# Kernel optimization log

Hardware: AMD Instinct MI355X
Metric: run time of the kernel (lower is better)

The kernel has to match this reference:

```python
import jax, jax.numpy as jnp
import numpy as np

N = 100000   # nodes
E = 1600000  # edges
IN = 32      # in_channels
ED = 16      # edge_dim
G = 128      # num graphs in batch
NEG = 0.01   # LeakyReLU default slope

def lrelu(v):
    return jnp.where(v > 0, v, NEG * v)

def gine_conv(x, src, dst, edge_attr, We, be, Wa, ba, Wb, bb):
    # PyG GINEConv (eps=0): out = nn(x + sum_{j->i} relu(x_j + lin(edge_attr)))
    e = edge_attr @ We + be                      # [E, d]
    m = jax.nn.relu(x[src] + e)                  # gather + add + relu
    agg = jax.ops.segment_sum(m, dst, num_segments=x.shape[0])
    h = x + agg
    return lrelu(h @ Wa + ba) @ Wb + bb

def setup_inputs() -> dict:
    key = jax.random.key(0)
    ks = jax.random.split(key, 24)
    w = lambda k, shape: (jax.random.normal(k, shape, dtype=jnp.float32) * 0.05)
    inp = {
        "x": jax.random.normal(ks[0], (N, IN), dtype=jnp.float32),
        "edge_index": jax.random.randint(ks[1], (2, E), 0, N),
        "edge_attr": jax.random.normal(ks[2], (E, ED), dtype=jnp.float32),
        "batch": jnp.sort(jax.random.randint(ks[3], (N,), 0, G)),
        # conv1: edge lin ED->IN, nn IN->32->64
        "We1": w(ks[4], (ED, IN)), "be1": w(ks[5], (IN,)),
        "W1a": w(ks[6], (IN, 32)), "b1a": w(ks[7], (32,)),
        "W1b": w(ks[8], (32, 64)), "b1b": w(ks[9], (64,)),
        # conv2: edge lin ED->64, nn 64->128->256
        "We2": w(ks[10], (ED, 64)), "be2": w(ks[11], (64,)),
        "W2a": w(ks[12], (64, 128)), "b2a": w(ks[13], (128,)),
        "W2b": w(ks[14], (128, 256)), "b2b": w(ks[15], (256,)),
        # head
        "Wf0": w(ks[16], (256, 128)), "bf0": w(ks[17], (128,)),
        "Wf1": w(ks[18], (128, 64)), "bf1": w(ks[19], (64,)),
        "Wf2": w(ks[20], (64, 32)), "bf2": w(ks[21], (32,)),
        "Wr": w(ks[22], (32, 1)), "br": w(ks[23], (1,)),
    }
    return inp

def reference(x, edge_index, edge_attr, batch,
              We1, be1, W1a, b1a, W1b, b1b,
              We2, be2, W2a, b2a, W2b, b2b,
              Wf0, bf0, Wf1, bf1, Wf2, bf2, Wr, br):
    src, dst = edge_index[0], edge_index[1]
    h = gine_conv(x, src, dst, edge_attr, We1, be1, W1a, b1a, W1b, b1b)
    h = lrelu(h)
    h = gine_conv(h, src, dst, edge_attr, We2, be2, W2a, b2a, W2b, b2b)
    h = lrelu(h)
    # global_add_pool over graph ids
    g = jax.ops.segment_sum(h, batch, num_segments=G)   # [G, 256]
    g = lrelu(g @ Wf0 + bf0)
    # dropout: identity (inference reference)
    g = lrelu(g @ Wf1 + bf1)
    g = lrelu(g @ Wf2 + bf2)
    out = (g @ Wr + br)[:, 0]                           # squeeze(dim=1)
    return out
```

## Files before the change

### kernel.cpp

```cpp
#include <hip/hip_runtime.h>

__device__ __forceinline__ float lrelu(float v){ return v > 0.f ? v : 0.01f*v; }

typedef __attribute__((ext_vector_type(8))) short v8s;
typedef __attribute__((ext_vector_type(4))) float v4f;

__device__ __forceinline__ unsigned short f2bf(float f){
    union{float f; unsigned int i;} v; v.f = f;
    unsigned int u = v.i;
    return (unsigned short)((u + 0x7fffu + ((u >> 16) & 1u)) >> 16);
}
__device__ __forceinline__ unsigned int pack2(float a, float b){
    return (unsigned int)f2bf(a) | ((unsigned int)f2bf(b) << 16);
}
__device__ __forceinline__ float bflo(unsigned int u){
    union{unsigned int i; float f;} v; v.i = u << 16; return v.f;
}
__device__ __forceinline__ float bfhi(unsigned int u){
    union{unsigned int i; float f;} v; v.i = u & 0xffff0000u; return v.f;
}
__device__ __forceinline__ float bf2f(unsigned short s){
    union{unsigned int i; float f;} v; v.i = ((unsigned int)s) << 16; return v.f;
}

__global__ __launch_bounds__(256) void k_hist(
    const int* __restrict__ ei, int* __restrict__ deg, int E)
{
    int e = blockIdx.x * 256 + threadIdx.x;
    if (e >= E) return;
    atomicAdd(&deg[ei[E + e]], 1);
}

__global__ __launch_bounds__(256) void k_scan1(
    const int* __restrict__ deg, int* __restrict__ rowptr,
    int* __restrict__ bsum, int N)
{
    __shared__ int sh[256];
    int t = threadIdx.x;
    int i = blockIdx.x * 256 + t;
    int v = (i < N) ? deg[i] : 0;
    sh[t] = v;
    __syncthreads();
    #pragma unroll
    for (int off = 1; off < 256; off <<= 1) {
        int add = (t >= off) ? sh[t - off] : 0;
        __syncthreads();
        sh[t] += add;
        __syncthreads();
    }
    if (i < N) rowptr[i] = sh[t] - v;
    if (t == 255) bsum[blockIdx.x] = sh[t];
}

__global__ __launch_bounds__(512) void k_scan2(int* __restrict__ bsum, int nb)
{
    __shared__ int sh[512];
    int t = threadIdx.x;
    int v = (t < nb) ? bsum[t] : 0;
    sh[t] = v;
    __syncthreads();
    #pragma unroll
    for (int off = 1; off < 512; off <<= 1) {
        int add = (t >= off) ? sh[t - off] : 0;
        __syncthreads();
        sh[t] += add;
        __syncthreads();
    }
    if (t < nb) bsum[t] = sh[t] - v;
}

__global__ __launch_bounds__(256) void k_scan3(
    int* __restrict__ rowptr, int* __restrict__ cursor,
    const int* __restrict__ bsum, int N)
{
    int i = blockIdx.x * 256 + threadIdx.x;
    if (i >= N) return;
    int rp = rowptr[i] + bsum[i >> 8];
    rowptr[i] = rp;
    cursor[i] = rp;
}

__global__ __launch_bounds__(256) void k_castx(
    const float* __restrict__ x, unsigned int* __restrict__ xb, int M8)
{
    int i = blockIdx.x * 256 + threadIdx.x;
    if (i >= M8) return;
    const float4* p = reinterpret_cast<const float4*>(x) + (size_t)i * 2;
    float4 a = p[0], b = p[1];
    uint4 o;
    o.x = pack2(a.x, a.y); o.y = pack2(a.z, a.w);
    o.z = pack2(b.x, b.y); o.w = pack2(b.z, b.w);
    reinterpret_cast<uint4*>(xb)[i] = o;
}

__global__ __launch_bounds__(256) void k_castw(
    const float* __restrict__ W2a, const float* __restrict__ W2b,
    const float* __restrict__ We1, const float* __restrict__ We2,
    unsigned short* __restrict__ W2aT, unsigned short* __restrict__ W2bT,
    unsigned short* __restrict__ WeT1, unsigned short* __restrict__ WeT2)
{
    int i = blockIdx.x * 256 + threadIdx.x;
    if (i < 128 * 64) {
        int n = i >> 6, k = i & 63;
        W2aT[i] = f2bf(W2a[k * 128 + n]);
    }
    int j = i - 128 * 64;
    if (j >= 0 && j < 256 * 128) {
        int n = j >> 7, k = j & 127;
        W2bT[j] = f2bf(W2b[k * 256 + n]);
    }
    int q1 = i - (128 * 64 + 256 * 128);
    if (q1 >= 0 && q1 < 32 * 32) {
        int cch = q1 >> 5, k = q1 & 31;
        WeT1[q1] = (k < 16) ? f2bf(We1[k * 32 + cch]) : (unsigned short)0;
    }
    int q2 = q1 - 32 * 32;
    if (q2 >= 0 && q2 < 64 * 32) {
        int cch = q2 >> 5, k = q2 & 31;
        WeT2[q2] = (k < 16) ? f2bf(We2[k * 64 + cch]) : (unsigned short)0;
    }
}

__global__ __launch_bounds__(256) void k_scatter(
    const int* __restrict__ ei, const float* __restrict__ ea,
    int* __restrict__ cursor, int2* __restrict__ csr2,
    uint4* __restrict__ eab, int E)
{
    int e = blockIdx.x * 256 + threadIdx.x;
    if (e >= E) return;
    int s = ei[e];
    int d = ei[E + e];
    int slot = atomicAdd(&cursor[d], 1);
    const float4* p = reinterpret_cast<const float4*>(ea) + (size_t)e * 4;
    float4 a = p[0], b = p[1], c = p[2], f = p[3];
    uint4 o0, o1;
    o0.x = pack2(a.x, a.y); o0.y = pack2(a.z, a.w);
    o0.z = pack2(b.x, b.y); o0.w = pack2(b.z, b.w);
    o1.x = pack2(c.x, c.y); o1.y = pack2(c.z, c.w);
    o1.z = pack2(f.x, f.y); o1.w = pack2(f.z, f.w);
    eab[(size_t)slot * 2]     = o0;
    eab[(size_t)slot * 2 + 1] = o1;
    int2 r; r.x = s; r.y = d;
    csr2[slot] = r;
}

#define AGG_SPW 64

__global__ __launch_bounds__(256) void k_agg2(
    const unsigned short* __restrict__ xb,
    const uint4* __restrict__ eab,
    const unsigned short* __restrict__ WeT,
    const float* __restrict__ be,
    const int2* __restrict__ csr2, float* __restrict__ agg, int E)
{
    __shared__ __align__(16) float lds[4][2][16][68];
    const int tid  = threadIdx.x;
    const int wv   = tid >> 6;
    const int lane = tid & 63;
    const int lid  = lane & 15;
    const int quad = lane >> 4;
    const int wave = __builtin_amdgcn_readfirstlane((blockIdx.x * 256 + tid) >> 6);
    const int s0 = wave * AGG_SPW;
    if (s0 >= E) return;
    const int nsl = (s0 + AGG_SPW <= E) ? AGG_SPW : E - s0;

    v8s af0 = *reinterpret_cast<const v8s*>(WeT + lid * 32 + quad * 8);
    v8s af1 = *reinterpret_cast<const v8s*>(WeT + (16 + lid) * 32 + quad * 8);
    v8s af2 = *reinterpret_cast<const v8s*>(WeT + (32 + lid) * 32 + quad * 8);
    v8s af3 = *reinterpret_cast<const v8s*>(WeT + (48 + lid) * 32 + quad * 8);
    const float biasc = be[lane];
    const int2*  cp = csr2 + s0;
    const uint4* ep = eab + (size_t)s0 * 2;

    unsigned short xv[2][16];
    int dsv[2][16];
    float acc = 0.f;
    int   cur = cp[0].y;
    bool  owned = false;

    auto GATHER = [&](int t) {
        const int base = t * 16;
        const int cnt = nsl - base;
        #pragma unroll
        for (int e = 0; e < 16; ++e) {
            int ee = (e < cnt) ? e : cnt - 1;
            int2 r = cp[base + ee];
            dsv[t & 1][e] = r.y;
            xv[t & 1][e] = xb[(unsigned)r.x * 64u + (unsigned)lane];
        }
    };
    auto MFMA = [&](int t) {
        int sl = t * 16 + lid;
        if (sl > nsl - 1) sl = nsl - 1;
        uint4 bw = {0u, 0u, 0u, 0u};
        if (quad < 2) bw = ep[2 * sl + quad];
        union { uint4 u; v8s s; } uu; uu.u = bw;
        v8s bf = uu.s;
        v4f d0 = {0.f, 0.f, 0.f, 0.f}, d1 = d0, d2 = d0, d3 = d0;
        d0 = __builtin_amdgcn_mfma_f32_16x16x32_bf16(af0, bf, d0, 0, 0, 0);
        d1 = __builtin_amdgcn_mfma_f32_16x16x32_bf16(af1, bf, d1, 0, 0, 0);
        d2 = __builtin_amdgcn_mfma_f32_16x16x32_bf16(af2, bf, d2, 0, 0, 0);
        d3 = __builtin_amdgcn_mfma_f32_16x16x32_bf16(af3, bf, d3, 0, 0, 0);
        float* lp = &lds[wv][t & 1][lid][quad * 4];
        *reinterpret_cast<v4f*>(lp)      = d0;
        *reinterpret_cast<v4f*>(lp + 16) = d1;
        *reinterpret_cast<v4f*>(lp + 32) = d2;
        *reinterpret_cast<v4f*>(lp + 48) = d3;
    };
    auto ACCUM = [&](int t) {
        const int cnt = nsl - t * 16;
        #pragma unroll
        for (int e = 0; e < 16; ++e) {
            if (e < cnt) {
                float ls = lds[wv][t & 1][e][lane];
                float m = ls + biasc + bf2f(xv[t & 1][e]);
                m = m > 0.f ? m : 0.f;
                int d = dsv[t & 1][e];
                if (d != cur) {
                    if (owned) agg[(unsigned)cur * 64u + lane] = acc;
                    else       atomicAdd(&agg[(unsigned)cur * 64u + lane], acc);
                    acc = 0.f; cur = d; owned = true;
                }
                acc += m;
            }
        }
    };

    GATHER(0); MFMA(0);
    #pragma unroll
    for (int t = 0; t < 4; ++t) {
        if (t * 16 < nsl) {
            if ((t + 1) < 4 && (t + 1) * 16 < nsl) { GATHER(t + 1); MFMA(t + 1); }
            ACCUM(t);
        }
    }
    atomicAdd(&agg[(unsigned)cur * 64u + lane], acc);
}

__global__ __launch_bounds__(256) void k_agg1(
    const unsigned short* __restrict__ xb,
    const uint4* __restrict__ eab,
    const unsigned short* __restrict__ WeT,
    const float* __restrict__ be,
    const int2* __restrict__ csr2, float* __restrict__ agg, int E)
{
    __shared__ __align__(16) float lds[4][2][16][36];
    const int tid  = threadIdx.x;
    const int wv   = tid >> 6;
    const int lane = tid & 63;
    const int lid  = lane & 15;
    const int quad = lane >> 4;
    const int c    = lane & 31;
    const int sub  = lane >> 5;
    const int wave = __builtin_amdgcn_readfirstlane((blockIdx.x * 256 + tid) >> 6);
    const int s0 = wave * AGG_SPW;
    if (s0 >= E) return;
    const int nsl = (s0 + AGG_SPW <= E) ? AGG_SPW : E - s0;

    v8s af0 = *reinterpret_cast<const v8s*>(WeT + lid * 32 + quad * 8);
    v8s af1 = *reinterpret_cast<const v8s*>(WeT + (16 + lid) * 32 + quad * 8);
    const float biasc = be[c];
    const int2*  cp = csr2 + s0;
    const uint4* ep = eab + (size_t)s0 * 2;

    unsigned short xv[2][8];
    int dsv[2][8];
    float acc = 0.f;
    int cur = cp[(sub < nsl) ? sub : 0].y;

    auto GATHER = [&](int t) {
        #pragma unroll
        for (int i = 0; i < 8; ++i) {
            int e = t * 16 + 2 * i + sub;
            int ee = (e < nsl) ? e : nsl - 1;
            int2 r = cp[ee];
            dsv[t & 1][i] = r.y;
            xv[t & 1][i] = xb[(unsigned)r.x * 32u + (unsigned)c];
        }
    };
    auto MFMA = [&](int t) {
        int sl = t * 16 + lid;
        if (sl > nsl - 1) sl = nsl - 1;
        uint4 bw = {0u, 0u, 0u, 0u};
        if (quad < 2) bw = ep[2 * sl + quad];
        union { uint4 u; v8s s; } uu; uu.u = bw;
        v8s bf = uu.s;
        v4f d0 = {0.f, 0.f, 0.f, 0.f}, d1 = d0;
        d0 = __builtin_amdgcn_mfma_f32_16x16x32_bf16(af0, bf, d0, 0, 0, 0);
        d1 = __builtin_amdgcn_mfma_f32_16x16x32_bf16(af1, bf, d1, 0, 0, 0);
        float* lp = &lds[wv][t & 1][lid][quad * 4];
        *reinterpret_cast<v4f*>(lp)      = d0;
        *reinterpret_cast<v4f*>(lp + 16) = d1;
    };
    auto ACCUM = [&](int t) {
        #pragma unroll
        for (int i = 0; i < 8; ++i) {
            int e = t * 16 + 2 * i + sub;
            if (e < nsl) {
                float ls = lds[wv][t & 1][2 * i + sub][c];
                float m = ls + biasc + bf2f(xv[t & 1][i]);
                m = m > 0.f ? m : 0.f;
                int d = dsv[t & 1][i];
                if (d != cur) {
                    atomicAdd(&agg[(unsigned)cur * 32u + c], acc);
                    acc = 0.f; cur = d;
                }
                acc += m;
            }
        }
    };

    GATHER(0); MFMA(0);
    #pragma unroll
    for (int t = 0; t < 4; ++t) {
        if (t * 16 < nsl) {
            if ((t + 1) < 4 && (t + 1) * 16 < nsl) { GATHER(t + 1); MFMA(t + 1); }
            ACCUM(t);
        }
    }
    atomicAdd(&agg[(unsigned)cur * 32u + c], acc);
}

__global__ __launch_bounds__(256, 4) void k_mlp1(
    const float* __restrict__ x, const float* __restrict__ agg1,
    const float* __restrict__ W1a, const float* __restrict__ b1a,
    const float* __restrict__ W1b, const float* __restrict__ b1b,
    unsigned int* __restrict__ h1b, int N)
{
    __shared__ float ts[64][33];
    const int tid = threadIdx.x;
    const int n0 = blockIdx.x * 64;
    const int row = tid & 63;
    const int grp = __builtin_amdgcn_readfirstlane(tid >> 6);
    const int g = n0 + row;

    float hv[32];
    if (g < N) {
        const float4* xp = reinterpret_cast<const float4*>(x) + (size_t)g * 8;
        const float4* ap = reinterpret_cast<const float4*>(agg1) + (size_t)g * 8;
        #pragma unroll
        for (int q = 0; q < 8; ++q) {
            float4 a = xp[q], b = ap[q];
            hv[4*q+0]=a.x+b.x; hv[4*q+1]=a.y+b.y;
            hv[4*q+2]=a.z+b.z; hv[4*q+3]=a.w+b.w;
        }
    } else {
        #pragma unroll
        for (int q = 0; q < 32; ++q) hv[q] = 0.f;
    }

    {
        const int c0 = grp * 8;
        float acc[8];
        #pragma unroll
        for (int i = 0; i < 8; ++i) acc[i] = b1a[c0 + i];
        for (int k = 0; k < 32; ++k) {
            float h = hv[k];
            const float* w = W1a + k*32 + c0;
            #pragma unroll
            for (int i = 0; i < 8; ++i) acc[i] = fmaf(h, w[i], acc[i]);
        }
        #pragma unroll
        for (int i = 0; i < 8; ++i) ts[row][c0 + i] = lrelu(acc[i]);
    }
    __syncthreads();

    {
        const int c0 = grp * 16;
        float acc[16];
        #pragma unroll
        for (int i = 0; i < 16; ++i) acc[i] = b1b[c0 + i];
        for (int k = 0; k < 32; ++k) {
            float tv = ts[row][k];
            const float* w = W1b + k*64 + c0;
            #pragma unroll
            for (int i = 0; i < 16; ++i) acc[i] = fmaf(tv, w[i], acc[i]);
        }
        if (g < N) {
            #pragma unroll
            for (int i = 0; i < 16; ++i) acc[i] = lrelu(acc[i]);
            uint4 p0, p1;
            p0.x = pack2(acc[0],  acc[1]);  p0.y = pack2(acc[2],  acc[3]);
            p0.z = pack2(acc[4],  acc[5]);  p0.w = pack2(acc[6],  acc[7]);
            p1.x = pack2(acc[8],  acc[9]);  p1.y = pack2(acc[10], acc[11]);
            p1.z = pack2(acc[12], acc[13]); p1.w = pack2(acc[14], acc[15]);
            uint4* bp = reinterpret_cast<uint4*>(h1b + (size_t)g*32 + (c0>>1));
            bp[0] = p0; bp[1] = p1;
        }
    }
}

__global__ __launch_bounds__(256) void k_mlp2(
    const unsigned int* __restrict__ h1b, const float* __restrict__ agg2,
    const unsigned short* __restrict__ W2aT, const float* __restrict__ b2a,
    const unsigned short* __restrict__ W2bT, const float* __restrict__ b2b,
    unsigned short* __restrict__ h2b, int N)
{
    __shared__ unsigned short hs[64][72];
    __shared__ unsigned short ts[64][136];
    const int tid = threadIdx.x;
    const int n0 = blockIdx.x * 64;

    {
        int r = tid >> 2, cseg = (tid & 3) * 16;
        int g = n0 + r;
        uint4 o0 = {0,0,0,0}, o1 = {0,0,0,0};
        if (g < N) {
            const uint4* hp = reinterpret_cast<const uint4*>(
                                  h1b + (size_t)g*32 + (cseg>>1));
            const float4* ap = reinterpret_cast<const float4*>(agg2)
                               + (size_t)g*16 + (cseg>>2);
            uint4 u0 = hp[0], u1 = hp[1];
            float4 b0=ap[0], b1=ap[1], b2=ap[2], b3=ap[3];
            o0.x = pack2(bflo(u0.x)+b0.x, bfhi(u0.x)+b0.y);
            o0.y = pack2(bflo(u0.y)+b0.z, bfhi(u0.y)+b0.w);
            o0.z = pack2(bflo(u0.z)+b1.x, bfhi(u0.z)+b1.y);
            o0.w = pack2(bflo(u0.w)+b1.z, bfhi(u0.w)+b1.w);
            o1.x = pack2(bflo(u1.x)+b2.x, bfhi(u1.x)+b2.y);
            o1.y = pack2(bflo(u1.y)+b2.z, bfhi(u1.y)+b2.w);
            o1.z = pack2(bflo(u1.z)+b3.x, bfhi(u1.z)+b3.y);
            o1.w = pack2(bflo(u1.w)+b3.z, bfhi(u1.w)+b3.w);
        }
        uint4* dp = reinterpret_cast<uint4*>(&hs[r][cseg]);
        dp[0] = o0; dp[1] = o1;
    }
    __syncthreads();

    const int wv   = __builtin_amdgcn_readfirstlane(tid >> 6);
    const int lane = tid & 63;
    const int lid  = lane & 15;
    const int quad = lane >> 4;

    v8s afA0 = *reinterpret_cast<const v8s*>(&hs[wv*16 + lid][quad*8]);
    v8s afA1 = *reinterpret_cast<const v8s*>(&hs[wv*16 + lid][32 + quad*8]);
    #pragma unroll
    for (int nt = 0; nt < 8; ++nt) {
        v4f acc = {0.f, 0.f, 0.f, 0.f};
        const unsigned short* wp = W2aT + (nt*16 + lid)*64 + quad*8;
        v8s b0 = *reinterpret_cast<const v8s*>(wp);
        v8s b1 = *reinterpret_cast<const v8s*>(wp + 32);
        acc = __builtin_amdgcn_mfma_f32_16x16x32_bf16(afA0, b0, acc, 0, 0, 0);
        acc = __builtin_amdgcn_mfma_f32_16x16x32_bf16(afA1, b1, acc, 0, 0, 0);
        float bias = b2a[nt*16 + lid];
        #pragma unroll
        for (int i = 0; i < 4; ++i) {
            float v = lrelu(acc[i] + bias);
            ts[wv*16 + quad*4 + i][nt*16 + lid] = f2bf(v);
        }
    }
    __syncthreads();

    v8s afB[4];
    #pragma unroll
    for (int ks = 0; ks < 4; ++ks)
        afB[ks] = *reinterpret_cast<const v8s*>(&ts[wv*16 + lid][ks*32 + quad*8]);
    const int gbase = n0 + wv*16 + quad*4;
    #pragma unroll 4
    for (int nt = 0; nt < 16; ++nt) {
        v4f acc = {0.f, 0.f, 0.f, 0.f};
        const unsigned short* wp = W2bT + (nt*16 + lid)*128 + quad*8;
        #pragma unroll
        for (int ks = 0; ks < 4; ++ks) {
            v8s bf = *reinterpret_cast<const v8s*>(wp + ks*32);
            acc = __builtin_amdgcn_mfma_f32_16x16x32_bf16(afB[ks], bf, acc, 0, 0, 0);
        }
        float bias = b2b[nt*16 + lid];
        #pragma unroll
        for (int i = 0; i < 4; ++i) {
            int g = gbase + i;
            if (g < N) {
                float v = lrelu(acc[i] + bias);
                h2b[(size_t)g*256 + nt*16 + lid] = f2bf(v);
            }
        }
    }
}

__global__ __launch_bounds__(256) void k_pool(
    const unsigned int* __restrict__ h2b, const int* __restrict__ batch,
    float* __restrict__ g, int N)
{
    int tid = threadIdx.x;
    int c2 = tid & 127;
    int h = tid >> 7;
    int base = blockIdx.x * 128;
    int n0 = base + h;
    int nend = base + 128; if (nend > N) nend = N;
    if (n0 >= N) return;
    float acc0 = 0.f, acc1 = 0.f;
    int cur = batch[n0];
    for (int n = n0; n < nend; n += 2) {
        int b = batch[n];
        unsigned int hv = h2b[(size_t)n * 128 + c2];
        if (b != cur) {
            atomicAdd(&g[(unsigned)cur * 256 + 2*c2],     acc0);
            atomicAdd(&g[(unsigned)cur * 256 + 2*c2 + 1], acc1);
            acc0 = acc1 = 0.f; cur = b;
        }
        acc0 += bflo(hv); acc1 += bfhi(hv);
    }
    atomicAdd(&g[(unsigned)cur * 256 + 2*c2],     acc0);
    atomicAdd(&g[(unsigned)cur * 256 + 2*c2 + 1], acc1);
}

__global__ __launch_bounds__(256) void k_head(
    const float* __restrict__ g,
    const float* __restrict__ Wf0, const float* __restrict__ bf0,
    const float* __restrict__ Wf1, const float* __restrict__ bf1,
    const float* __restrict__ Wf2, const float* __restrict__ bf2,
    const float* __restrict__ Wr,  const float* __restrict__ br,
    float* __restrict__ out)
{
    __shared__ float buf[256];
    __shared__ float t0[128];
    __shared__ float t1[64];
    __shared__ float t2[32];
    int gid = blockIdx.x, tid = threadIdx.x;
    buf[tid] = g[(size_t)gid*256 + tid];
    __syncthreads();
    if (tid < 128) {
        float acc = bf0[tid];
        for (int k = 0; k < 256; ++k) acc = fmaf(buf[k], Wf0[k*128 + tid], acc);
        t0[tid] = lrelu(acc);
    }
    __syncthreads();
    if (tid < 64) {
        float acc = bf1[tid];
        for (int k = 0; k < 128; ++k) acc = fmaf(t0[k], Wf1[k*64 + tid], acc);
        t1[tid] = lrelu(acc);
    }
    __syncthreads();
    if (tid < 32) {
        float acc = bf2[tid];
        for (int k = 0; k < 64; ++k) acc = fmaf(t1[k], Wf2[k*32 + tid], acc);
        t2[tid] = lrelu(acc);
    }
    __syncthreads();
    if (tid == 0) {
        float acc = br[0];
        for (int k = 0; k < 32; ++k) acc = fmaf(t2[k], Wr[k], acc);
        out[gid] = acc;
    }
}

extern "C" void kernel_launch(void* const* d_in, const int* in_sizes, int n_in,
                              void* d_out, int out_size, void* d_ws, size_t ws_size,
                              hipStream_t stream)
{
    const float* x     = (const float*)d_in[0];
    const int*   ei    = (const int*)d_in[1];
    const float* ea    = (const float*)d_in[2];
    const int*   batch = (const int*)d_in[3];
    const float* We1=(const float*)d_in[4],  *be1=(const float*)d_in[5];
    const float* W1a=(const float*)d_in[6],  *b1a=(const float*)d_in[7];
    const float* W1b=(const float*)d_in[8],  *b1b=(const float*)d_in[9];
    const float* We2=(const float*)d_in[10], *be2=(const float*)d_in[11];
    const float* W2a=(const float*)d_in[12], *b2a=(const float*)d_in[13];
    const float* W2b=(const float*)d_in[14], *b2b=(const float*)d_in[15];
    const float* Wf0=(const float*)d_in[16], *bf0=(const float*)d_in[17];
    const float* Wf1=(const float*)d_in[18], *bf1=(const float*)d_in[19];
    const float* Wf2=(const float*)d_in[20], *bf2=(const float*)d_in[21];
    const float* Wr =(const float*)d_in[22], *br =(const float*)d_in[23];

    const int N = in_sizes[0] / 32;
    const int E = in_sizes[1] / 2;
    const int G = out_size;
    const int nb = (N + 255) / 256;
    const int nb64 = (N + 63) / 64;

    char* p = (char*)d_ws;
    int*   deg     = (int*)p;                 p += (size_t)N * 4;
    float* gbuf    = (float*)p;               p += (size_t)G * 256 * 4;
    float* agg1    = (float*)p;               p += (size_t)N * 32 * 4;
    float* agg2    = (float*)p;               p += (size_t)N * 64 * 4;
    size_t zero_bytes = (size_t)(p - (char*)d_ws);
    int*   rowptr  = (int*)p;                 p += (size_t)N * 4;
    int*   cursor  = (int*)p;                 p += (size_t)N * 4;
    int*   bsum    = (int*)p;                 p += 512 * 4;
    p = (char*)(((uintptr_t)p + 63) & ~(uintptr_t)63);
    int2*  csr2    = (int2*)p;                p += (size_t)E * 8;
    uint4* eab     = (uint4*)p;               p += (size_t)E * 32;
    unsigned short* xb   = (unsigned short*)p; p += (size_t)N * 32 * 2;
    unsigned int*   h1b  = (unsigned int*)p;  p += (size_t)N * 64 * 2;
    unsigned short* W2aT = (unsigned short*)p; p += 128 * 64 * 2;
    unsigned short* W2bT = (unsigned short*)p; p += 256 * 128 * 2;
    unsigned short* WeT1 = (unsigned short*)p; p += 32 * 32 * 2;
    unsigned short* WeT2 = (unsigned short*)p; p += 64 * 32 * 2;
    unsigned short* h2b  = (unsigned short*)p; p += (size_t)N * 256 * 2;

    hipMemsetAsync(d_ws, 0, zero_bytes, stream);

    int eb = (E + 255) / 256;

    k_hist   <<<eb, 256, 0, stream>>>(ei, deg, E);
    k_scan1  <<<nb, 256, 0, stream>>>(deg, rowptr, bsum, N);
    k_scan2  <<<1, 512, 0, stream>>>(bsum, nb);
    k_scan3  <<<nb, 256, 0, stream>>>(rowptr, cursor, bsum, N);
    {
        int M8 = N * 32 / 8;
        k_castx<<<(M8 + 255) / 256, 256, 0, stream>>>(x, (unsigned int*)xb, M8);
    }
    {
        int tot = 128*64 + 256*128 + 32*32 + 64*32;
        k_castw<<<(tot + 255) / 256, 256, 0, stream>>>(W2a, W2b, We1, We2,
                                                       W2aT, W2bT, WeT1, WeT2);
    }
    k_scatter<<<eb, 256, 0, stream>>>(ei, ea, cursor, csr2, eab, E);

    {
        int waves = (E + AGG_SPW - 1) / AGG_SPW;
        int blocks = (waves + 3) / 4;
        k_agg1<<<blocks, 256, 0, stream>>>(xb, eab, WeT1, be1, csr2, agg1, E);
    }
    k_mlp1<<<nb64, 256, 0, stream>>>(x, agg1, W1a, b1a, W1b, b1b,
                                     (unsigned int*)h1b, N);

    {
        int waves = (E + AGG_SPW - 1) / AGG_SPW;
        int blocks = (waves + 3) / 4;
        k_agg2<<<blocks, 256, 0, stream>>>((const unsigned short*)h1b, eab, WeT2,
                                           be2, csr2, agg2, E);
    }
    k_mlp2<<<nb64, 256, 0, stream>>>(h1b, agg2, W2aT, b2a, W2bT, b2b, h2b, N);

    k_pool<<<(N + 127) / 128, 256, 0, stream>>>((const unsigned int*)h2b, batch,
                                                gbuf, N);
    k_head<<<G, 256, 0, stream>>>(gbuf, Wf0, bf0, Wf1, bf1, Wf2, bf2, Wr, br,
                                  (float*)d_out);
}
```

Measured before the change: 624.8 us.

## Fuse global add pooling into second MLP kernel via shared-memory atomics

Removes the k_pool kernel and the N×256 bf16 h2b intermediate. k_mlp2 now accumulates its lrelu outputs per graph into a small shared-memory pool covering up to four graph ids starting at the block's first batch id. It falls back to global atomics for other ids, then flushes the shared pool to gbuf with global atomics. This saves roughly 51 MB of writes and reads plus one launch, at the cost of many shared-memory atomics inside the MFMA loop.

```diff
diff --git a/kernel.cpp b/kernel.cpp
--- a/kernel.cpp
+++ b/kernel.cpp
@@ -394,14 +394,18 @@
     const unsigned int* __restrict__ h1b, const float* __restrict__ agg2,
     const unsigned short* __restrict__ W2aT, const float* __restrict__ b2a,
     const unsigned short* __restrict__ W2bT, const float* __restrict__ b2b,
-    unsigned short* __restrict__ h2b, int N)
+    const int* __restrict__ batch, float* __restrict__ gbuf, int N, int G)
 {
     __shared__ unsigned short hs[64][72];
     __shared__ unsigned short ts[64][136];
+    __shared__ float pool[4][260];
     const int tid = threadIdx.x;
     const int n0 = blockIdx.x * 64;
+    const int bmin = batch[n0];
 
     {
+        #pragma unroll
+        for (int r = 0; r < 4; ++r) pool[r][tid] = 0.f;
         int r = tid >> 2, cseg = (tid & 3) * 16;
         int g = n0 + r;
         uint4 o0 = {0,0,0,0}, o1 = {0,0,0,0};
@@ -455,6 +459,12 @@
     for (int ks = 0; ks < 4; ++ks)
         afB[ks] = *reinterpret_cast<const v8s*>(&ts[wv*16 + lid][ks*32 + quad*8]);
     const int gbase = n0 + wv*16 + quad*4;
+    int pb[4];
+    #pragma unroll
+    for (int i = 0; i < 4; ++i) {
+        int g = gbase + i;
+        pb[i] = (g < N) ? batch[g] : -1;
+    }
     #pragma unroll 4
     for (int nt = 0; nt < 16; ++nt) {
         v4f acc = {0.f, 0.f, 0.f, 0.f};
@@ -467,40 +477,24 @@
         float bias = b2b[nt*16 + lid];
         #pragma unroll
         for (int i = 0; i < 4; ++i) {
-            int g = gbase + i;
-            if (g < N) {
+            if (pb[i] >= 0) {
                 float v = lrelu(acc[i] + bias);
-                h2b[(size_t)g*256 + nt*16 + lid] = f2bf(v);
+                int idx = pb[i] - bmin;
+                if (idx < 4) atomicAdd(&pool[idx][nt*16 + lid], v);
+                else atomicAdd(&gbuf[(size_t)pb[i]*256 + nt*16 + lid], v);
             }
         }
     }
-}
-
-__global__ __launch_bounds__(256) void k_pool(
-    const unsigned int* __restrict__ h2b, const int* __restrict__ batch,
-    float* __restrict__ g, int N)
-{
-    int tid = threadIdx.x;
-    int c2 = tid & 127;
-    int h = tid >> 7;
-    int base = blockIdx.x * 128;
-    int n0 = base + h;
-    int nend = base + 128; if (nend > N) nend = N;
-    if (n0 >= N) return;
-    float acc0 = 0.f, acc1 = 0.f;
-    int cur = batch[n0];
-    for (int n = n0; n < nend; n += 2) {
-        int b = batch[n];
-        unsigned int hv = h2b[(size_t)n * 128 + c2];
-        if (b != cur) {
-            atomicAdd(&g[(unsigned)cur * 256 + 2*c2],     acc0);
-            atomicAdd(&g[(unsigned)cur * 256 + 2*c2 + 1], acc1);
-            acc0 = acc1 = 0.f; cur = b;
-        }
-        acc0 += bflo(hv); acc1 += bfhi(hv);
-    }
-    atomicAdd(&g[(unsigned)cur * 256 + 2*c2],     acc0);
-    atomicAdd(&g[(unsigned)cur * 256 + 2*c2 + 1], acc1);
+    __syncthreads();
+
+    #pragma unroll
+    for (int r = 0; r < 4; ++r) {
+        int gr = bmin + r;
+        if (gr < G) {
+            float v = pool[r][tid];
+            if (v != 0.f) atomicAdd(&gbuf[(size_t)gr*256 + tid], v);
+        }
+    }
 }
 
 __global__ __launch_bounds__(256) void k_head(
@@ -586,7 +580,6 @@
     unsigned short* W2bT = (unsigned short*)p; p += 256 * 128 * 2;
     unsigned short* WeT1 = (unsigned short*)p; p += 32 * 32 * 2;
     unsigned short* WeT2 = (unsigned short*)p; p += 64 * 32 * 2;
-    unsigned short* h2b  = (unsigned short*)p; p += (size_t)N * 256 * 2;
 
     hipMemsetAsync(d_ws, 0, zero_bytes, stream);
 
@@ -621,10 +614,9 @@
         k_agg2<<<blocks, 256, 0, stream>>>((const unsigned short*)h1b, eab, WeT2,
                                            be2, csr2, agg2, E);
     }
-    k_mlp2<<<nb64, 256, 0, stream>>>(h1b, agg2, W2aT, b2a, W2bT, b2b, h2b, N);
-
-    k_pool<<<(N + 127) / 128, 256, 0, stream>>>((const unsigned int*)h2b, batch,
-                                                gbuf, N);
+    k_mlp2<<<nb64, 256, 0, stream>>>(h1b, agg2, W2aT, b2a, W2bT, b2b,
+                                     batch, gbuf, N, G);
+
     k_head<<<G, 256, 0, stream>>>(gbuf, Wf0, bf0, Wf1, bf1, Wf2, bf2, Wr, br,
                                   (float*)d_out);
 }
```

Result: slower. 683.9 us (+9.5%).
